# Kernel tuning notes

Measured on AMD Instinct MI355X. Metric: run time of the kernel, lower is better.

Reference implementation:

```python
import jax, jax.numpy as jnp
import numpy as np

ALPHA = 1.0  # config.cnet_alpha


def setup_inputs() -> dict:
    key = jax.random.key(0)
    k1, k2 = jax.random.split(key)
    z = jax.random.normal(k1, (8192, 2048), dtype=jnp.float32)
    centroids = jax.random.normal(k2, (512, 2048), dtype=jnp.float32)
    return {"z": z, "centroids": centroids}


def reference(z, centroids):
    # --- compute_similarity, 'EUC' branch ---
    # torch: sqrt(sum((z[None] - centroids[:, None])**2, dim=2)).T
    # computed here via the expanded quadratic form (same math, no
    # (n_clusters, bs, n_hidden) materialization):
    z_sq = jnp.sum(z * z, axis=1, keepdims=True)              # (bs, 1)
    c_sq = jnp.sum(centroids * centroids, axis=1)[None, :]    # (1, n_clusters)
    cross = jnp.einsum('bh,ch->bc', z, centroids)             # (bs, n_clusters)
    d2 = jnp.maximum(z_sq + c_sq - 2.0 * cross, 0.0)
    similarity = jnp.sqrt(d2)                                 # (bs, n_clusters)

    # --- Student-t soft assignment Q ---
    Q = jnp.power(1.0 + similarity / ALPHA, -(ALPHA + 1.0) / 2.0)
    Q = Q / jnp.nansum(Q, axis=1, keepdims=True)

    # --- target distribution P ---
    P = (Q * Q) / jnp.sum(Q, axis=0, keepdims=True)
    P = P / jnp.nansum(P, axis=1, keepdims=True)

    return jnp.stack([Q, P])  # (2, bs, n_clusters)
```

## Files before the change

### kernel.cpp

```cpp
#include <hip/hip_runtime.h>
#include <stdint.h>

#define M_ROWS 8192
#define NCLUST 512
#define KDIM   2048

#define BM 256
#define BN 256
#define BKB 128
#define KSPLIT 4
#define NKT (KDIM / KSPLIT / BKB)

typedef __attribute__((ext_vector_type(4))) int   i32x4;
typedef __attribute__((ext_vector_type(8))) int   i32x8;
typedef __attribute__((ext_vector_type(4))) float f32x4;
typedef __attribute__((ext_vector_type(8))) unsigned short u16x8;

__device__ __forceinline__ unsigned short f2bf(float f) {
    unsigned u = __float_as_uint(f);
    u += 0x7FFFu + ((u >> 16) & 1u);
    return (unsigned short)(u >> 16);
}
__device__ __forceinline__ float bf2f(unsigned short h) {
    return __uint_as_float(((unsigned)h) << 16);
}

__device__ __forceinline__ void gload_lds16(const void* g, void* l) {
    __builtin_amdgcn_global_load_lds(
        (const __attribute__((address_space(1))) void*)g,
        (__attribute__((address_space(3))) void*)l,
        16, 0, 0);
}

__global__ __launch_bounds__(256) void k_convert(
    const float* __restrict__ z, const float* __restrict__ cent,
    unsigned char* __restrict__ zb, unsigned char* __restrict__ cb,
    float* __restrict__ zsq, float* __restrict__ csq,
    float* __restrict__ colsum)
{
    int w = threadIdx.x >> 6, lane = threadIdx.x & 63;
    int row = blockIdx.x * 4 + w;

    const float* src;
    unsigned char* dst;
    float* nrm;
    int r;
    if (row < M_ROWS) { src = z + (size_t)row * KDIM; dst = zb + (size_t)row * KDIM; nrm = zsq; r = row; }
    else              { r = row - M_ROWS; src = cent + (size_t)r * KDIM; dst = cb + (size_t)r * KDIM; nrm = csq; }

    float s = 0.f;
    #pragma unroll
    for (int it = 0; it < KDIM / 256; ++it) {
        int idx = it * 256 + lane * 4;
        float4 v = *(const float4*)(src + idx);
        s += v.x * v.x + v.y * v.y + v.z * v.z + v.w * v.w;
        int p = __builtin_amdgcn_cvt_pk_fp8_f32(v.x, v.y, 0, 0);
        p     = __builtin_amdgcn_cvt_pk_fp8_f32(v.z, v.w, p, 1);
        *(int*)(dst + idx) = p;
    }
    #pragma unroll
    for (int off = 32; off; off >>= 1) s += __shfl_down(s, off);
    if (lane == 0) nrm[r] = s;

    if (blockIdx.x == 0) {
        colsum[threadIdx.x] = 0.f;
        colsum[threadIdx.x + 256] = 0.f;
    }
}

__global__ __launch_bounds__(512, 2) void k_gemm_part(
    const unsigned char* __restrict__ zb, const unsigned char* __restrict__ cb,
    unsigned short* __restrict__ parts)
{
    __shared__ unsigned char As[2][BM * BKB];
    __shared__ unsigned char Bs[2][BN * BKB];

    const int wgid = blockIdx.x;
    const int by   = wgid & 31;
    const int rest = wgid >> 5;
    const int bx   = rest & 1;
    const int bz   = rest >> 1;
    const int bRow = by * BM;
    const int bCol = bx * BN;
    const size_t kb0 = (size_t)bz * (KDIM / KSPLIT);

    const int tid  = threadIdx.x;
    const int w    = tid >> 6, lane = tid & 63;
    const int wrow = w >> 2, wcol = w & 3;

    f32x4 acc[8][4] = {};

    const int srow = lane >> 3;
    const int scol = ((lane & 7) ^ srow) * 16;
    const unsigned char* gA = zb + (size_t)(bRow + srow) * KDIM + kb0 + scol;
    const unsigned char* gB = cb + (size_t)(bCol + srow) * KDIM + kb0 + scol;

    auto stage = [&](int buf, int kt) {
        const int kb = kt * BKB;
        #pragma unroll
        for (int j = 0; j < 4; ++j) {
            const int g = w * 4 + j;
            gload_lds16(gA + (size_t)(g * 8) * KDIM + kb, &As[buf][g * 1024]);
            gload_lds16(gB + (size_t)(g * 8) * KDIM + kb, &Bs[buf][g * 1024]);
        }
    };

    const int arowb = wrow * 128 + (lane & 15);
    const int bcolb = wcol * 64 + (lane & 15);
    const int s     = lane >> 4;
    const int r7    = lane & 7;
    const int sc    = 0x7F7F7F7F;

    auto compute = [&](int buf) {
        const unsigned char* A0 = &As[buf][0];
        const unsigned char* B0 = &Bs[buf][0];
        i32x8 af[8];
        #pragma unroll
        for (int i = 0; i < 8; ++i) {
            const int row = arowb + i * 16;
            const i32x4 lo = *(const i32x4*)&A0[row * BKB + ((2 * s) ^ r7) * 16];
            const i32x4 hi = *(const i32x4*)&A0[row * BKB + ((2 * s + 1) ^ r7) * 16];
            af[i][0] = lo[0]; af[i][1] = lo[1]; af[i][2] = lo[2]; af[i][3] = lo[3];
            af[i][4] = hi[0]; af[i][5] = hi[1]; af[i][6] = hi[2]; af[i][7] = hi[3];
        }
        #pragma unroll
        for (int j = 0; j < 4; ++j) {
            const int row = bcolb + j * 16;
            const i32x4 lo = *(const i32x4*)&B0[row * BKB + ((2 * s) ^ r7) * 16];
            const i32x4 hi = *(const i32x4*)&B0[row * BKB + ((2 * s + 1) ^ r7) * 16];
            i32x8 bf;
            bf[0] = lo[0]; bf[1] = lo[1]; bf[2] = lo[2]; bf[3] = lo[3];
            bf[4] = hi[0]; bf[5] = hi[1]; bf[6] = hi[2]; bf[7] = hi[3];
            #pragma unroll
            for (int i = 0; i < 8; ++i)
                acc[i][j] = __builtin_amdgcn_mfma_scale_f32_16x16x128_f8f6f4(
                    af[i], bf, acc[i][j], 0, 0, 0, sc, 0, sc);
        }
    };

    stage(0, 0);
    __syncthreads();
    int buf = 0;
    for (int kt = 0; kt < NKT - 1; ++kt) {
        stage(buf ^ 1, kt + 1);
        compute(buf);
        __syncthreads();
        buf ^= 1;
    }
    compute(buf);

    unsigned short* dst = parts + (size_t)bz * M_ROWS * NCLUST;
    const int col0 = bCol + wcol * 64 + (lane & 15);
    const int row0 = bRow + wrow * 128 + (lane >> 4) * 4;
    #pragma unroll
    for (int j = 0; j < 4; ++j) {
        const int col = col0 + j * 16;
        #pragma unroll
        for (int i = 0; i < 8; ++i)
            #pragma unroll
            for (int r = 0; r < 4; ++r)
                dst[(size_t)(row0 + i * 128 / 8 + r) * NCLUST + col] = f2bf(acc[i][j][r]);
    }
}

__global__ __launch_bounds__(256) void k_q_norm(
    const unsigned short* __restrict__ parts,
    const float* __restrict__ zsq, const float* __restrict__ csq,
    float* __restrict__ Q, float* __restrict__ colsum)
{
    __shared__ float red[4][NCLUST];
    const int tid = threadIdx.x, w = tid >> 6, lane = tid & 63;
    const size_t PSTR = (size_t)M_ROWS * NCLUST;
    float ca[8] = {0, 0, 0, 0, 0, 0, 0, 0};
    const int rbase = blockIdx.x * 32;

    float cs[8];
    {
        float4 c0 = *(const float4*)(csq + lane * 8);
        float4 c1 = *(const float4*)(csq + lane * 8 + 4);
        cs[0] = c0.x; cs[1] = c0.y; cs[2] = c0.z; cs[3] = c0.w;
        cs[4] = c1.x; cs[5] = c1.y; cs[6] = c1.z; cs[7] = c1.w;
    }

    for (int rr = 0; rr < 8; ++rr) {
        const int row = rbase + w + rr * 4;
        const size_t off = (size_t)row * NCLUST + lane * 8;
        float x[8] = {0, 0, 0, 0, 0, 0, 0, 0};
        #pragma unroll
        for (int p = 0; p < KSPLIT; ++p) {
            u16x8 v = *(const u16x8*)(parts + p * PSTR + off);
            #pragma unroll
            for (int k = 0; k < 8; ++k) x[k] += bf2f(v[k]);
        }
        const float zr = zsq[row];
        float q[8];
        float sum = 0.f;
        #pragma unroll
        for (int k = 0; k < 8; ++k) {
            q[k] = 1.0f / (1.0f + sqrtf(fmaxf(zr + cs[k] - 2.0f * x[k], 0.0f)));
            sum += q[k];
        }
        #pragma unroll
        for (int o = 32; o; o >>= 1) sum += __shfl_down(sum, o);
        sum = __shfl(sum, 0);
        const float inv = 1.0f / sum;
        float4 q0, q1;
        q0.x = q[0] * inv; q0.y = q[1] * inv; q0.z = q[2] * inv; q0.w = q[3] * inv;
        q1.x = q[4] * inv; q1.y = q[5] * inv; q1.z = q[6] * inv; q1.w = q[7] * inv;
        *(float4*)(Q + off)     = q0;
        *(float4*)(Q + off + 4) = q1;
        ca[0] += q0.x; ca[1] += q0.y; ca[2] += q0.z; ca[3] += q0.w;
        ca[4] += q1.x; ca[5] += q1.y; ca[6] += q1.z; ca[7] += q1.w;
    }
    #pragma unroll
    for (int c = 0; c < 8; ++c) red[w][lane * 8 + c] = ca[c];
    __syncthreads();
    const float t0 = red[0][tid] + red[1][tid] + red[2][tid] + red[3][tid];
    const float t1 = red[0][tid + 256] + red[1][tid + 256] + red[2][tid + 256] + red[3][tid + 256];
    atomicAdd(&colsum[tid], t0);
    atomicAdd(&colsum[tid + 256], t1);
}

__global__ __launch_bounds__(256) void k_p(
    const float* __restrict__ Q, const float* __restrict__ colsum,
    float* __restrict__ P)
{
    const int w = threadIdx.x >> 6, lane = threadIdx.x & 63;
    const int row = blockIdx.x * 4 + w;
    const float* qp = Q + (size_t)row * NCLUST;
    float4 q0 = *(const float4*)(qp + lane * 4);
    float4 q1 = *(const float4*)(qp + 256 + lane * 4);
    float4 c0 = *(const float4*)(colsum + lane * 4);
    float4 c1 = *(const float4*)(colsum + 256 + lane * 4);
    float4 p0, p1;
    p0.x = q0.x * q0.x / c0.x; p0.y = q0.y * q0.y / c0.y;
    p0.z = q0.z * q0.z / c0.z; p0.w = q0.w * q0.w / c0.w;
    p1.x = q1.x * q1.x / c1.x; p1.y = q1.y * q1.y / c1.y;
    p1.z = q1.z * q1.z / c1.z; p1.w = q1.w * q1.w / c1.w;
    float s = p0.x + p0.y + p0.z + p0.w + p1.x + p1.y + p1.z + p1.w;
    #pragma unroll
    for (int off = 32; off; off >>= 1) s += __shfl_down(s, off);
    s = __shfl(s, 0);
    const float inv = 1.0f / s;
    p0.x *= inv; p0.y *= inv; p0.z *= inv; p0.w *= inv;
    p1.x *= inv; p1.y *= inv; p1.z *= inv; p1.w *= inv;
    float* op = P + (size_t)row * NCLUST;
    *(float4*)(op + lane * 4) = p0;
    *(float4*)(op + 256 + lane * 4) = p1;
}

extern "C" void kernel_launch(void* const* d_in, const int* in_sizes, int n_in,
                              void* d_out, int out_size, void* d_ws, size_t ws_size,
                              hipStream_t stream) {
    const float* z    = (const float*)d_in[0];
    const float* cent = (const float*)d_in[1];
    float* out = (float*)d_out;

    char* ws = (char*)d_ws;
    unsigned char* zb = (unsigned char*)ws;
    unsigned char* cb = (unsigned char*)(ws + 16777216);
    float* zsq    = (float*)(ws + 17825792);
    float* csq    = (float*)(ws + 17858560);
    float* colsum = (float*)(ws + 17860608);
    unsigned short* parts = (unsigned short*)(ws + 18874368);

    float* Q = out;
    float* P = out + (size_t)M_ROWS * NCLUST;

    k_convert<<<dim3((M_ROWS + NCLUST) / 4), dim3(256), 0, stream>>>(
        z, cent, zb, cb, zsq, csq, colsum);

    k_gemm_part<<<dim3(256), dim3(512), 0, stream>>>(zb, cb, parts);

    k_q_norm<<<dim3(M_ROWS / 32), dim3(256), 0, stream>>>(
        parts, zsq, csq, Q, colsum);

    k_p<<<dim3(M_ROWS / 4), dim3(256), 0, stream>>>(Q, colsum, P);
}
```

Before: 66.31 us.

## Restructure FP8 GEMM main loop with single barrier, explicit waitcnt and interleaved MFMA

```diff
diff --git a/kernel.cpp b/kernel.cpp
--- a/kernel.cpp
+++ b/kernel.cpp
@@ -111,43 +111,57 @@
     const int r7    = lane & 7;
     const int sc    = 0x7F7F7F7F;
 
-    auto compute = [&](int buf) {
+    stage(0, 0);
+
+    #pragma unroll
+    for (int t = 0; t < NKT; ++t) {
+        const int buf = t & 1;
+        __builtin_amdgcn_s_barrier();
+        if (t + 1 < NKT) {
+            stage(buf ^ 1, t + 1);
+            asm volatile("s_waitcnt vmcnt(8)" ::: "memory");
+        } else {
+            asm volatile("s_waitcnt vmcnt(0)" ::: "memory");
+        }
+        __builtin_amdgcn_sched_barrier(0);
+
         const unsigned char* A0 = &As[buf][0];
         const unsigned char* B0 = &Bs[buf][0];
-        i32x8 af[8];
-        #pragma unroll
-        for (int i = 0; i < 8; ++i) {
-            const int row = arowb + i * 16;
-            const i32x4 lo = *(const i32x4*)&A0[row * BKB + ((2 * s) ^ r7) * 16];
-            const i32x4 hi = *(const i32x4*)&A0[row * BKB + ((2 * s + 1) ^ r7) * 16];
-            af[i][0] = lo[0]; af[i][1] = lo[1]; af[i][2] = lo[2]; af[i][3] = lo[3];
-            af[i][4] = hi[0]; af[i][5] = hi[1]; af[i][6] = hi[2]; af[i][7] = hi[3];
-        }
+
+        i32x8 bf[4];
         #pragma unroll
         for (int j = 0; j < 4; ++j) {
             const int row = bcolb + j * 16;
             const i32x4 lo = *(const i32x4*)&B0[row * BKB + ((2 * s) ^ r7) * 16];
             const i32x4 hi = *(const i32x4*)&B0[row * BKB + ((2 * s + 1) ^ r7) * 16];
-            i32x8 bf;
-            bf[0] = lo[0]; bf[1] = lo[1]; bf[2] = lo[2]; bf[3] = lo[3];
-            bf[4] = hi[0]; bf[5] = hi[1]; bf[6] = hi[2]; bf[7] = hi[3];
-            #pragma unroll
-            for (int i = 0; i < 8; ++i)
-                acc[i][j] = __builtin_amdgcn_mfma_scale_f32_16x16x128_f8f6f4(
-                    af[i], bf, acc[i][j], 0, 0, 0, sc, 0, sc);
-        }
-    };
-
-    stage(0, 0);
-    __syncthreads();
-    int buf = 0;
-    for (int kt = 0; kt < NKT - 1; ++kt) {
-        stage(buf ^ 1, kt + 1);
-        compute(buf);
-        __syncthreads();
-        buf ^= 1;
-    }
-    compute(buf);
+            bf[j][0] = lo[0]; bf[j][1] = lo[1]; bf[j][2] = lo[2]; bf[j][3] = lo[3];
+            bf[j][4] = hi[0]; bf[j][5] = hi[1]; bf[j][6] = hi[2]; bf[j][7] = hi[3];
+        }
+
+        #pragma unroll
+        for (int q = 0; q < 4; ++q) {
+            i32x8 af[2];
+            #pragma unroll
+            for (int ii = 0; ii < 2; ++ii) {
+                const int row = arowb + (q * 2 + ii) * 16;
+                const i32x4 lo = *(const i32x4*)&A0[row * BKB + ((2 * s) ^ r7) * 16];
+                const i32x4 hi = *(const i32x4*)&A0[row * BKB + ((2 * s + 1) ^ r7) * 16];
+                af[ii][0] = lo[0]; af[ii][1] = lo[1]; af[ii][2] = lo[2]; af[ii][3] = lo[3];
+                af[ii][4] = hi[0]; af[ii][5] = hi[1]; af[ii][6] = hi[2]; af[ii][7] = hi[3];
+            }
+            asm volatile("s_waitcnt lgkmcnt(0)" ::: "memory");
+            __builtin_amdgcn_sched_barrier(0);
+            __builtin_amdgcn_s_setprio(1);
+            #pragma unroll
+            for (int ii = 0; ii < 2; ++ii)
+                #pragma unroll
+                for (int j = 0; j < 4; ++j)
+                    acc[q * 2 + ii][j] = __builtin_amdgcn_mfma_scale_f32_16x16x128_f8f6f4(
+                        af[ii], bf[j], acc[q * 2 + ii][j], 0, 0, 0, sc, 0, sc);
+            __builtin_amdgcn_s_setprio(0);
+            __builtin_amdgcn_sched_barrier(0);
+        }
+    }
 
     unsigned short* dst = parts + (size_t)bz * M_ROWS * NCLUST;
     const int col0 = bCol + wcol * 64 + (lane & 15);
@@ -159,7 +173,7 @@
         for (int i = 0; i < 8; ++i)
             #pragma unroll
             for (int r = 0; r < 4; ++r)
-                dst[(size_t)(row0 + i * 128 / 8 + r) * NCLUST + col] = f2bf(acc[i][j][r]);
+                dst[(size_t)(row0 + i * 16 + r) * NCLUST + col] = f2bf(acc[i][j][r]);
     }
 }
 
```

After: 65.79 us. About the same (-0.8%).

## Fuse FP8 GEMM with Q computation and row normalization in one kernel

Applied to the files above, without the earlier changes.

```diff
diff --git a/kernel.cpp b/kernel.cpp
--- a/kernel.cpp
+++ b/kernel.cpp
@@ -5,25 +5,12 @@
 #define NCLUST 512
 #define KDIM   2048
 
-#define BM 256
-#define BN 256
-#define BKB 128
-#define KSPLIT 4
-#define NKT (KDIM / KSPLIT / BKB)
+#define BM    32
+#define NSTEP (KDIM / 128)
 
 typedef __attribute__((ext_vector_type(4))) int   i32x4;
 typedef __attribute__((ext_vector_type(8))) int   i32x8;
 typedef __attribute__((ext_vector_type(4))) float f32x4;
-typedef __attribute__((ext_vector_type(8))) unsigned short u16x8;
-
-__device__ __forceinline__ unsigned short f2bf(float f) {
-    unsigned u = __float_as_uint(f);
-    u += 0x7FFFu + ((u >> 16) & 1u);
-    return (unsigned short)(u >> 16);
-}
-__device__ __forceinline__ float bf2f(unsigned short h) {
-    return __uint_as_float(((unsigned)h) << 16);
-}
 
 __device__ __forceinline__ void gload_lds16(const void* g, void* l) {
     __builtin_amdgcn_global_load_lds(
@@ -68,157 +55,138 @@
     }
 }
 
-__global__ __launch_bounds__(512, 2) void k_gemm_part(
+__global__ __launch_bounds__(1024, 4) void k_gemm_fused(
     const unsigned char* __restrict__ zb, const unsigned char* __restrict__ cb,
-    unsigned short* __restrict__ parts)
-{
-    __shared__ unsigned char As[2][BM * BKB];
-    __shared__ unsigned char Bs[2][BN * BKB];
-
-    const int wgid = blockIdx.x;
-    const int by   = wgid & 31;
-    const int rest = wgid >> 5;
-    const int bx   = rest & 1;
-    const int bz   = rest >> 1;
-    const int bRow = by * BM;
-    const int bCol = bx * BN;
-    const size_t kb0 = (size_t)bz * (KDIM / KSPLIT);
-
-    const int tid  = threadIdx.x;
-    const int w    = tid >> 6, lane = tid & 63;
-    const int wrow = w >> 2, wcol = w & 3;
-
-    f32x4 acc[8][4] = {};
-
-    const int srow = lane >> 3;
-    const int scol = ((lane & 7) ^ srow) * 16;
-    const unsigned char* gA = zb + (size_t)(bRow + srow) * KDIM + kb0 + scol;
-    const unsigned char* gB = cb + (size_t)(bCol + srow) * KDIM + kb0 + scol;
-
-    auto stage = [&](int buf, int kt) {
-        const int kb = kt * BKB;
-        #pragma unroll
-        for (int j = 0; j < 4; ++j) {
-            const int g = w * 4 + j;
-            gload_lds16(gA + (size_t)(g * 8) * KDIM + kb, &As[buf][g * 1024]);
-            gload_lds16(gB + (size_t)(g * 8) * KDIM + kb, &Bs[buf][g * 1024]);
-        }
-    };
-
-    const int arowb = wrow * 128 + (lane & 15);
-    const int bcolb = wcol * 64 + (lane & 15);
-    const int s     = lane >> 4;
-    const int r7    = lane & 7;
-    const int sc    = 0x7F7F7F7F;
-
-    auto compute = [&](int buf) {
-        const unsigned char* A0 = &As[buf][0];
-        const unsigned char* B0 = &Bs[buf][0];
-        i32x8 af[8];
-        #pragma unroll
-        for (int i = 0; i < 8; ++i) {
-            const int row = arowb + i * 16;
-            const i32x4 lo = *(const i32x4*)&A0[row * BKB + ((2 * s) ^ r7) * 16];
-            const i32x4 hi = *(const i32x4*)&A0[row * BKB + ((2 * s + 1) ^ r7) * 16];
-            af[i][0] = lo[0]; af[i][1] = lo[1]; af[i][2] = lo[2]; af[i][3] = lo[3];
-            af[i][4] = hi[0]; af[i][5] = hi[1]; af[i][6] = hi[2]; af[i][7] = hi[3];
-        }
-        #pragma unroll
-        for (int j = 0; j < 4; ++j) {
-            const int row = bcolb + j * 16;
-            const i32x4 lo = *(const i32x4*)&B0[row * BKB + ((2 * s) ^ r7) * 16];
-            const i32x4 hi = *(const i32x4*)&B0[row * BKB + ((2 * s + 1) ^ r7) * 16];
-            i32x8 bf;
-            bf[0] = lo[0]; bf[1] = lo[1]; bf[2] = lo[2]; bf[3] = lo[3];
-            bf[4] = hi[0]; bf[5] = hi[1]; bf[6] = hi[2]; bf[7] = hi[3];
-            #pragma unroll
-            for (int i = 0; i < 8; ++i)
-                acc[i][j] = __builtin_amdgcn_mfma_scale_f32_16x16x128_f8f6f4(
-                    af[i], bf, acc[i][j], 0, 0, 0, sc, 0, sc);
-        }
-    };
-
-    stage(0, 0);
-    __syncthreads();
-    int buf = 0;
-    for (int kt = 0; kt < NKT - 1; ++kt) {
-        stage(buf ^ 1, kt + 1);
-        compute(buf);
-        __syncthreads();
-        buf ^= 1;
-    }
-    compute(buf);
-
-    unsigned short* dst = parts + (size_t)bz * M_ROWS * NCLUST;
-    const int col0 = bCol + wcol * 64 + (lane & 15);
-    const int row0 = bRow + wrow * 128 + (lane >> 4) * 4;
-    #pragma unroll
-    for (int j = 0; j < 4; ++j) {
-        const int col = col0 + j * 16;
-        #pragma unroll
-        for (int i = 0; i < 8; ++i)
-            #pragma unroll
-            for (int r = 0; r < 4; ++r)
-                dst[(size_t)(row0 + i * 128 / 8 + r) * NCLUST + col] = f2bf(acc[i][j][r]);
-    }
-}
-
-__global__ __launch_bounds__(256) void k_q_norm(
-    const unsigned short* __restrict__ parts,
     const float* __restrict__ zsq, const float* __restrict__ csq,
     float* __restrict__ Q, float* __restrict__ colsum)
 {
-    __shared__ float red[4][NCLUST];
-    const int tid = threadIdx.x, w = tid >> 6, lane = tid & 63;
-    const size_t PSTR = (size_t)M_ROWS * NCLUST;
-    float ca[8] = {0, 0, 0, 0, 0, 0, 0, 0};
-    const int rbase = blockIdx.x * 32;
-
-    float cs[8];
-    {
-        float4 c0 = *(const float4*)(csq + lane * 8);
-        float4 c1 = *(const float4*)(csq + lane * 8 + 4);
-        cs[0] = c0.x; cs[1] = c0.y; cs[2] = c0.z; cs[3] = c0.w;
-        cs[4] = c1.x; cs[5] = c1.y; cs[6] = c1.z; cs[7] = c1.w;
-    }
-
-    for (int rr = 0; rr < 8; ++rr) {
-        const int row = rbase + w + rr * 4;
-        const size_t off = (size_t)row * NCLUST + lane * 8;
-        float x[8] = {0, 0, 0, 0, 0, 0, 0, 0};
-        #pragma unroll
-        for (int p = 0; p < KSPLIT; ++p) {
-            u16x8 v = *(const u16x8*)(parts + p * PSTR + off);
+    __shared__ unsigned char As[BM * KDIM];
+    __shared__ float rws[BM][16];
+    __shared__ float rinv[BM];
+
+    const int tid  = threadIdx.x;
+    const int w    = tid >> 6, lane = tid & 63;
+    const int rbase = blockIdx.x * BM;
+    const int l15  = lane & 15;
+    const int s    = lane >> 4;
+
+    #pragma unroll
+    for (int t = 0; t < 4; ++t) {
+        const int row  = 2 * w + (t >> 1);
+        const int half = t & 1;
+        const unsigned char* src = zb + (size_t)(rbase + row) * KDIM
+            + half * 1024 + (lane >> 3) * 128 + (((lane & 7) ^ (row & 7)) * 16);
+        gload_lds16(src, &As[row * KDIM + half * 1024]);
+    }
+    __syncthreads();
+
+    f32x4 acc[2][2] = {};
+    const int sc = 0x7F7F7F7F;
+
+    const int colb = w * 32;
+    const unsigned char* bbase = cb + (size_t)(colb + l15) * KDIM + s * 32;
+
+    i32x4 bl[2][2][2];
+    #pragma unroll
+    for (int j = 0; j < 2; ++j) {
+        bl[0][j][0] = *(const i32x4*)(bbase + (size_t)j * 16 * KDIM);
+        bl[0][j][1] = *(const i32x4*)(bbase + (size_t)j * 16 * KDIM + 16);
+    }
+
+    #pragma unroll
+    for (int k = 0; k < NSTEP; ++k) {
+        const int cur = k & 1;
+        if (k + 1 < NSTEP) {
             #pragma unroll
-            for (int k = 0; k < 8; ++k) x[k] += bf2f(v[k]);
-        }
-        const float zr = zsq[row];
-        float q[8];
-        float sum = 0.f;
-        #pragma unroll
-        for (int k = 0; k < 8; ++k) {
-            q[k] = 1.0f / (1.0f + sqrtf(fmaxf(zr + cs[k] - 2.0f * x[k], 0.0f)));
-            sum += q[k];
-        }
-        #pragma unroll
-        for (int o = 32; o; o >>= 1) sum += __shfl_down(sum, o);
-        sum = __shfl(sum, 0);
-        const float inv = 1.0f / sum;
-        float4 q0, q1;
-        q0.x = q[0] * inv; q0.y = q[1] * inv; q0.z = q[2] * inv; q0.w = q[3] * inv;
-        q1.x = q[4] * inv; q1.y = q[5] * inv; q1.z = q[6] * inv; q1.w = q[7] * inv;
-        *(float4*)(Q + off)     = q0;
-        *(float4*)(Q + off + 4) = q1;
-        ca[0] += q0.x; ca[1] += q0.y; ca[2] += q0.z; ca[3] += q0.w;
-        ca[4] += q1.x; ca[5] += q1.y; ca[6] += q1.z; ca[7] += q1.w;
-    }
-    #pragma unroll
-    for (int c = 0; c < 8; ++c) red[w][lane * 8 + c] = ca[c];
+            for (int j = 0; j < 2; ++j) {
+                bl[cur ^ 1][j][0] = *(const i32x4*)(bbase + (size_t)j * 16 * KDIM + (k + 1) * 128);
+                bl[cur ^ 1][j][1] = *(const i32x4*)(bbase + (size_t)j * 16 * KDIM + (k + 1) * 128 + 16);
+            }
+        }
+        i32x8 af[2];
+        #pragma unroll
+        for (int i = 0; i < 2; ++i) {
+            const int row = i * 16 + l15;
+            const i32x4 lo = *(const i32x4*)&As[row * KDIM + k * 128 + (((2 * s)     ^ (row & 7)) * 16)];
+            const i32x4 hi = *(const i32x4*)&As[row * KDIM + k * 128 + (((2 * s + 1) ^ (row & 7)) * 16)];
+            af[i][0] = lo[0]; af[i][1] = lo[1]; af[i][2] = lo[2]; af[i][3] = lo[3];
+            af[i][4] = hi[0]; af[i][5] = hi[1]; af[i][6] = hi[2]; af[i][7] = hi[3];
+        }
+        #pragma unroll
+        for (int j = 0; j < 2; ++j) {
+            i32x8 bf;
+            bf[0] = bl[cur][j][0][0]; bf[1] = bl[cur][j][0][1];
+            bf[2] = bl[cur][j][0][2]; bf[3] = bl[cur][j][0][3];
+            bf[4] = bl[cur][j][1][0]; bf[5] = bl[cur][j][1][1];
+            bf[6] = bl[cur][j][1][2]; bf[7] = bl[cur][j][1][3];
+            #pragma unroll
+            for (int i = 0; i < 2; ++i)
+                acc[i][j] = __builtin_amdgcn_mfma_scale_f32_16x16x128_f8f6f4(
+                    af[i], bf, acc[i][j], 0, 0, 0, sc, 0, sc);
+        }
+    }
+
+    float csv[2];
+    csv[0] = csq[colb + l15];
+    csv[1] = csq[colb + 16 + l15];
+
+    float qv[2][2][4];
+    #pragma unroll
+    for (int i = 0; i < 2; ++i) {
+        #pragma unroll
+        for (int r = 0; r < 4; ++r) {
+            const float zr = zsq[rbase + i * 16 + s * 4 + r];
+            #pragma unroll
+            for (int j = 0; j < 2; ++j) {
+                const float d2 = zr + csv[j] - 2.0f * acc[i][j][r];
+                qv[i][j][r] = 1.0f / (1.0f + sqrtf(fmaxf(d2, 0.0f)));
+            }
+        }
+    }
+
+    #pragma unroll
+    for (int i = 0; i < 2; ++i) {
+        #pragma unroll
+        for (int r = 0; r < 4; ++r) {
+            float rp = qv[i][0][r] + qv[i][1][r];
+            rp += __shfl_xor(rp, 1);
+            rp += __shfl_xor(rp, 2);
+            rp += __shfl_xor(rp, 4);
+            rp += __shfl_xor(rp, 8);
+            if (l15 == 0) rws[i * 16 + s * 4 + r][w] = rp;
+        }
+    }
     __syncthreads();
-    const float t0 = red[0][tid] + red[1][tid] + red[2][tid] + red[3][tid];
-    const float t1 = red[0][tid + 256] + red[1][tid + 256] + red[2][tid + 256] + red[3][tid + 256];
-    atomicAdd(&colsum[tid], t0);
-    atomicAdd(&colsum[tid + 256], t1);
+    if (tid < BM) {
+        float ssum = 0.f;
+        #pragma unroll
+        for (int w2 = 0; w2 < 16; ++w2) ssum += rws[tid][w2];
+        rinv[tid] = 1.0f / ssum;
+    }
+    __syncthreads();
+
+    float cp0 = 0.f, cp1 = 0.f;
+    #pragma unroll
+    for (int i = 0; i < 2; ++i) {
+        #pragma unroll
+        for (int r = 0; r < 4; ++r) {
+            const int row = i * 16 + s * 4 + r;
+            const float ri = rinv[row];
+            const size_t off = (size_t)(rbase + row) * NCLUST + colb;
+            const float q0 = qv[i][0][r] * ri;
+            const float q1 = qv[i][1][r] * ri;
+            Q[off + l15]      = q0;
+            Q[off + 16 + l15] = q1;
+            cp0 += q0;
+            cp1 += q1;
+        }
+    }
+    cp0 += __shfl_xor(cp0, 16); cp0 += __shfl_xor(cp0, 32);
+    cp1 += __shfl_xor(cp1, 16); cp1 += __shfl_xor(cp1, 32);
+    if (s == 0) {
+        atomicAdd(&colsum[colb + l15], cp0);
+        atomicAdd(&colsum[colb + 16 + l15], cp1);
+    }
 }
 
 __global__ __launch_bounds__(256) void k_p(
@@ -262,7 +230,6 @@
     float* zsq    = (float*)(ws + 17825792);
     float* csq    = (float*)(ws + 17858560);
     float* colsum = (float*)(ws + 17860608);
-    unsigned short* parts = (unsigned short*)(ws + 18874368);
 
     float* Q = out;
     float* P = out + (size_t)M_ROWS * NCLUST;
@@ -270,10 +237,8 @@
     k_convert<<<dim3((M_ROWS + NCLUST) / 4), dim3(256), 0, stream>>>(
         z, cent, zb, cb, zsq, csq, colsum);
 
-    k_gemm_part<<<dim3(256), dim3(512), 0, stream>>>(zb, cb, parts);
-
-    k_q_norm<<<dim3(M_ROWS / 32), dim3(256), 0, stream>>>(
-        parts, zsq, csq, Q, colsum);
+    k_gemm_fused<<<dim3(M_ROWS / BM), dim3(1024), 0, stream>>>(
+        zb, cb, zsq, csq, Q, colsum);
 
     k_p<<<dim3(M_ROWS / 4), dim3(256), 0, stream>>>(Q, colsum, P);
 }
```

After: 72.09 us. 8.7% more time.

## Shrink GEMM tiles to 128x128, halve K-split, and remap block order

Applied to the files above, without the earlier changes.

```diff
diff --git a/kernel.cpp b/kernel.cpp
--- a/kernel.cpp
+++ b/kernel.cpp
@@ -5,10 +5,10 @@
 #define NCLUST 512
 #define KDIM   2048
 
-#define BM 256
-#define BN 256
+#define BM 128
+#define BN 128
 #define BKB 128
-#define KSPLIT 4
+#define KSPLIT 2
 #define NKT (KDIM / KSPLIT / BKB)
 
 typedef __attribute__((ext_vector_type(4))) int   i32x4;
@@ -68,7 +68,7 @@
     }
 }
 
-__global__ __launch_bounds__(512, 2) void k_gemm_part(
+__global__ __launch_bounds__(512) void k_gemm_part(
     const unsigned char* __restrict__ zb, const unsigned char* __restrict__ cb,
     unsigned short* __restrict__ parts)
 {
@@ -76,19 +76,19 @@
     __shared__ unsigned char Bs[2][BN * BKB];
 
     const int wgid = blockIdx.x;
-    const int by   = wgid & 31;
-    const int rest = wgid >> 5;
-    const int bx   = rest & 1;
-    const int bz   = rest >> 1;
+    const int inner = wgid >> 3;
+    const int bx  = inner & 3;
+    const int bz  = (inner >> 2) & 1;
+    const int by  = ((inner >> 3) << 3) | (wgid & 7);
     const int bRow = by * BM;
     const int bCol = bx * BN;
     const size_t kb0 = (size_t)bz * (KDIM / KSPLIT);
 
-    const int tid  = threadIdx.x;
-    const int w    = tid >> 6, lane = tid & 63;
-    const int wrow = w >> 2, wcol = w & 3;
-
-    f32x4 acc[8][4] = {};
+    const int tid  = threadIdx.x & 255;
+    const int w    = (threadIdx.x >> 6) & 3, lane = threadIdx.x & 63;
+    const int wr   = w >> 1,  wc   = w & 1;
+
+    f32x4 acc[4][4] = {};
 
     const int srow = lane >> 3;
     const int scol = ((lane & 7) ^ srow) * 16;
@@ -105,8 +105,8 @@
         }
     };
 
-    const int arowb = wrow * 128 + (lane & 15);
-    const int bcolb = wcol * 64 + (lane & 15);
+    const int arowb = wr * 64 + (lane & 15);
+    const int bcolb = wc * 64 + (lane & 15);
     const int s     = lane >> 4;
     const int r7    = lane & 7;
     const int sc    = 0x7F7F7F7F;
@@ -114,9 +114,9 @@
     auto compute = [&](int buf) {
         const unsigned char* A0 = &As[buf][0];
         const unsigned char* B0 = &Bs[buf][0];
-        i32x8 af[8];
-        #pragma unroll
-        for (int i = 0; i < 8; ++i) {
+        i32x8 af[4], bfr[4];
+        #pragma unroll
+        for (int i = 0; i < 4; ++i) {
             const int row = arowb + i * 16;
             const i32x4 lo = *(const i32x4*)&A0[row * BKB + ((2 * s) ^ r7) * 16];
             const i32x4 hi = *(const i32x4*)&A0[row * BKB + ((2 * s + 1) ^ r7) * 16];
@@ -128,14 +128,15 @@
             const int row = bcolb + j * 16;
             const i32x4 lo = *(const i32x4*)&B0[row * BKB + ((2 * s) ^ r7) * 16];
             const i32x4 hi = *(const i32x4*)&B0[row * BKB + ((2 * s + 1) ^ r7) * 16];
-            i32x8 bf;
-            bf[0] = lo[0]; bf[1] = lo[1]; bf[2] = lo[2]; bf[3] = lo[3];
-            bf[4] = hi[0]; bf[5] = hi[1]; bf[6] = hi[2]; bf[7] = hi[3];
+            bfr[j][0] = lo[0]; bfr[j][1] = lo[1]; bfr[j][2] = lo[2]; bfr[j][3] = lo[3];
+            bfr[j][4] = hi[0]; bfr[j][5] = hi[1]; bfr[j][6] = hi[2]; bfr[j][7] = hi[3];
+        }
+        #pragma unroll
+        for (int i = 0; i < 4; ++i)
             #pragma unroll
-            for (int i = 0; i < 8; ++i)
+            for (int j = 0; j < 4; ++j)
                 acc[i][j] = __builtin_amdgcn_mfma_scale_f32_16x16x128_f8f6f4(
-                    af[i], bf, acc[i][j], 0, 0, 0, sc, 0, sc);
-        }
+                    af[i], bfr[j], acc[i][j], 0, 0, 0, sc, 0, sc);
     };
 
     stage(0, 0);
@@ -150,17 +151,18 @@
     compute(buf);
 
     unsigned short* dst = parts + (size_t)bz * M_ROWS * NCLUST;
-    const int col0 = bCol + wcol * 64 + (lane & 15);
-    const int row0 = bRow + wrow * 128 + (lane >> 4) * 4;
+    const int col0 = bCol + wc * 64 + (lane & 15);
+    const int row0 = bRow + wr * 64 + (lane >> 4) * 4;
     #pragma unroll
     for (int j = 0; j < 4; ++j) {
         const int col = col0 + j * 16;
         #pragma unroll
-        for (int i = 0; i < 8; ++i)
+        for (int i = 0; i < 4; ++i)
             #pragma unroll
             for (int r = 0; r < 4; ++r)
-                dst[(size_t)(row0 + i * 128 / 8 + r) * NCLUST + col] = f2bf(acc[i][j][r]);
-    }
+                dst[(size_t)(row0 + i * 16 + r) * NCLUST + col] = f2bf(acc[i][j][r]);
+    }
+    (void)tid;
 }
 
 __global__ __launch_bounds__(256) void k_q_norm(
@@ -185,12 +187,12 @@
     for (int rr = 0; rr < 8; ++rr) {
         const int row = rbase + w + rr * 4;
         const size_t off = (size_t)row * NCLUST + lane * 8;
-        float x[8] = {0, 0, 0, 0, 0, 0, 0, 0};
-        #pragma unroll
-        for (int p = 0; p < KSPLIT; ++p) {
-            u16x8 v = *(const u16x8*)(parts + p * PSTR + off);
+        float x[8];
+        {
+            u16x8 v0 = *(const u16x8*)(parts + off);
+            u16x8 v1 = *(const u16x8*)(parts + PSTR + off);
             #pragma unroll
-            for (int k = 0; k < 8; ++k) x[k] += bf2f(v[k]);
+            for (int k = 0; k < 8; ++k) x[k] = bf2f(v0[k]) + bf2f(v1[k]);
         }
         const float zr = zsq[row];
         float q[8];
@@ -270,7 +272,7 @@
     k_convert<<<dim3((M_ROWS + NCLUST) / 4), dim3(256), 0, stream>>>(
         z, cent, zb, cb, zsq, csq, colsum);
 
-    k_gemm_part<<<dim3(256), dim3(512), 0, stream>>>(zb, cb, parts);
+    k_gemm_part<<<dim3(512), dim3(256), 0, stream>>>(zb, cb, parts);
 
     k_q_norm<<<dim3(M_ROWS / 32), dim3(256), 0, stream>>>(
         parts, zsq, csq, Q, colsum);
```

Measured after the change: 55.93 us. 15.6% less time.
